# Kernel tuning notes

Measured on AMD Instinct MI355X. Metric: run time of the kernel, lower is better.

## Reference

```python
import jax, jax.numpy as jnp
import numpy as np

EPS = 1e-12  # torch F.normalize default eps


def _l2norm(x):
    n = jnp.sqrt(jnp.sum(x * x, axis=-1, keepdims=True))
    return x / jnp.maximum(n, EPS)


def setup_inputs() -> dict:
    key = jax.random.key(0)
    ks = jax.random.split(key, 8)
    B, T, V = 4, 2048, 512
    C, H, NB = 512, 4, 64
    return {
        "x": jax.random.normal(ks[0], (B, T, V), dtype=jnp.float32),
        "basis": jax.random.normal(ks[1], (V, 2 * NB), dtype=jnp.float32),
        "shared_q_w": jax.random.normal(ks[2], (V, C), dtype=jnp.float32) * 0.02,
        "shared_k_w": jax.random.normal(ks[3], (V, C), dtype=jnp.float32) * 0.02,
        "v_coeffs": jax.random.normal(ks[4], (C, 2 * NB), dtype=jnp.float32) * 0.02,
        "o_coeffs": jax.random.normal(ks[5], (C, 2 * NB), dtype=jnp.float32) * 0.02,
        "decay_logits": jnp.linspace(1.0, 5.0, H, dtype=jnp.float32),
        "out_scale": jnp.float32(0.1),
    }


def reference(x, basis, shared_q_w, shared_k_w, v_coeffs, o_coeffs, decay_logits, out_scale):
    B, T, V = x.shape
    H = decay_logits.shape[0]
    C = shared_q_w.shape[1]
    D = C // H

    v_w = basis @ v_coeffs.T  # [V, C]
    o_w = basis @ o_coeffs.T  # [V, C]

    q = _l2norm(x @ shared_q_w)  # [B, T, C]
    k = _l2norm(x @ shared_k_w)
    v = x @ v_w

    # [B, H, T, D]
    q = q.reshape(B, T, H, D).transpose(0, 2, 1, 3)
    k = k.reshape(B, T, H, D).transpose(0, 2, 1, 3)
    v = v.reshape(B, T, H, D).transpose(0, 2, 1, 3)

    scores = jnp.einsum("bhqd,bhkd->bhqk", q, k)  # [B, H, T, T]

    decay = jax.nn.sigmoid(decay_logits)  # [H]
    pos = jnp.arange(T)
    diff = pos[None, :] - pos[:, None]  # diff[i, j] = j - i
    mask = (diff > 0).astype(scores.dtype)  # [T, T]
    expo = jnp.clip(diff.astype(jnp.float32) - 1.0, 0.0, None)  # [T, T]
    decay_w = (decay[:, None, None] ** expo[None]) * mask[None]  # [H, T, T]

    scores = scores * decay_w[None].astype(scores.dtype)
    retrieved = jnp.einsum("bhqk,bhkd->bhqd", scores, v)  # [B, H, T, D]
    retrieved = retrieved.transpose(0, 2, 1, 3).reshape(B, T, C)
    return retrieved @ o_w.T * out_scale  # [B, T, V]
```

## Files before the change

### kernel.cpp

```cpp
#include <hip/hip_runtime.h>
#include <hip/hip_bf16.h>

#define BB 4
#define TT 2048
#define VV 512
#define CC 512
#define HH 4
#define DD 128
#define NB2 128
#define NROWS (BB*TT)
#define QC 64
#define NCH (TT/QC)
#define SST 66
#define EPS 1e-12f

typedef __attribute__((ext_vector_type(8))) short bf16x8;
typedef __attribute__((ext_vector_type(4))) float f32x4;
typedef unsigned short u16;

__device__ __forceinline__ void gl_lds16(const void* g, void* l) {
    __builtin_amdgcn_global_load_lds(
        (const __attribute__((address_space(1))) unsigned int*)g,
        (__attribute__((address_space(3))) unsigned int*)l, 16, 0, 0);
}
__device__ __forceinline__ u16 f2bu(float x) {
    __hip_bfloat16 h = __float2bfloat16(x);
    return *reinterpret_cast<u16*>(&h);
}
__device__ __forceinline__ float bu2f(u16 u) {
    __hip_bfloat16 h = *reinterpret_cast<__hip_bfloat16*>(&u);
    return __bfloat162float(h);
}
__device__ __forceinline__ uint4 pack8(float4 a, float4 b, float s) {
    u16 h[8] = {f2bu(a.x * s), f2bu(a.y * s), f2bu(a.z * s), f2bu(a.w * s),
                f2bu(b.x * s), f2bu(b.y * s), f2bu(b.z * s), f2bu(b.w * s)};
    return *(uint4*)h;
}

#define P4_TR  512
#define P4_Z   16
#define P4_WG  32
__global__ __launch_bounds__(256) void prep_all4(
    const float* __restrict__ qw, const float* __restrict__ kw,
    const float* __restrict__ basis, const float* __restrict__ v_coeffs,
    const float* __restrict__ o_coeffs, const float* __restrict__ out_scale,
    u16* __restrict__ wq, u16* __restrict__ wk,
    u16* __restrict__ v_wT, u16* __restrict__ o_ws, float* __restrict__ norms)
{
    __shared__ __align__(16) union {
        float tile[32][33];
        struct { u16 A[4096]; u16 B[4096]; } w;
    } sm;
    const int bi = blockIdx.x, t = threadIdx.x;
    if (bi < P4_TR) {
        int id = bi;
        const int z = id >> 8; id &= 255;
        const float* in = z ? kw : qw;
        u16* outT = z ? wk : wq;
        const int bx = (id & 15) * 32, by = (id >> 4) * 32;
        const int tx = t & 31, ty = t >> 5;
        #pragma unroll
        for (int r = 0; r < 32; r += 8)
            sm.tile[ty + r][tx] = in[(size_t)(by + ty + r) * CC + bx + tx];
        __syncthreads();
        #pragma unroll
        for (int r = 0; r < 32; r += 8)
            outT[(size_t)(bx + ty + r) * VV + by + tx] = f2bu(sm.tile[tx][ty + r]);
    } else if (bi < P4_TR + P4_Z) {
        int idx = (bi - P4_TR) * 256 + t;
        ((float4*)norms)[idx] = make_float4(0.f, 0.f, 0.f, 0.f);
    } else {
        int id = bi - (P4_TR + P4_Z);
        const int sec = id >> 4, rem = id & 15;
        const int m0 = (rem >> 2) * 128, n0 = (rem & 3) * 128;
        const float* Af = sec ? basis : v_coeffs;
        const float* Bf = sec ? o_coeffs : basis;
        u16* Cp = sec ? o_ws : v_wT;
        const float scB = sec ? out_scale[0] : 1.f;
        const int wave = t >> 6, lane = t & 63;
        const int qq = lane >> 4, l16 = lane & 15;
        const int wm = (wave >> 1) * 64, wn = (wave & 1) * 64;
        const int s0 = wave * 128 + lane, s1 = s0 + 64;
        const int r0 = s0 >> 2, c0 = ((s0 & 3) - (r0 >> 1)) & 3;
        const int r1 = s1 >> 2, c1 = ((s1 & 3) - (r1 >> 1)) & 3;
        f32x4 acc[4][4];
        #pragma unroll
        for (int i = 0; i < 4; ++i)
            #pragma unroll
            for (int j = 0; j < 4; ++j) acc[i][j] = (f32x4){0.f, 0.f, 0.f, 0.f};
        for (int k0 = 0; k0 < NB2; k0 += 32) {
            __syncthreads();
            {
                const float* p0 = Af + (size_t)(m0 + r0) * NB2 + k0 + c0 * 8;
                const float* p1 = Af + (size_t)(m0 + r1) * NB2 + k0 + c1 * 8;
                *(uint4*)&sm.w.A[s0 * 8] = pack8(((const float4*)p0)[0], ((const float4*)p0)[1], 1.f);
                *(uint4*)&sm.w.A[s1 * 8] = pack8(((const float4*)p1)[0], ((const float4*)p1)[1], 1.f);
                const float* q0 = Bf + (size_t)(n0 + r0) * NB2 + k0 + c0 * 8;
                const float* q1 = Bf + (size_t)(n0 + r1) * NB2 + k0 + c1 * 8;
                *(uint4*)&sm.w.B[s0 * 8] = pack8(((const float4*)q0)[0], ((const float4*)q0)[1], scB);
                *(uint4*)&sm.w.B[s1 * 8] = pack8(((const float4*)q1)[0], ((const float4*)q1)[1], scB);
            }
            __syncthreads();
            bf16x8 af[4], bfr[4];
            #pragma unroll
            for (int mt = 0; mt < 4; ++mt) {
                const int r = wm + mt * 16 + l16;
                af[mt] = *(const bf16x8*)&sm.w.A[(r * 4 + ((qq + (r >> 1)) & 3)) * 8];
            }
            #pragma unroll
            for (int nt = 0; nt < 4; ++nt) {
                const int r = wn + nt * 16 + l16;
                bfr[nt] = *(const bf16x8*)&sm.w.B[(r * 4 + ((qq + (r >> 1)) & 3)) * 8];
            }
            #pragma unroll
            for (int mt = 0; mt < 4; ++mt)
                #pragma unroll
                for (int nt = 0; nt < 4; ++nt)
                    acc[mt][nt] = __builtin_amdgcn_mfma_f32_16x16x32_bf16(
                        af[mt], bfr[nt], acc[mt][nt], 0, 0, 0);
        }
        #pragma unroll
        for (int mt = 0; mt < 4; ++mt)
            #pragma unroll
            for (int rr = 0; rr < 4; ++rr) {
                int grow = m0 + wm + mt * 16 + qq * 4 + rr;
                #pragma unroll
                for (int nt = 0; nt < 4; ++nt)
                    Cp[(size_t)grow * 512 + n0 + wn + nt * 16 + l16] = f2bu(acc[mt][nt][rr]);
            }
    }
}

__global__ __launch_bounds__(256) void gemm_qkv3(
    const float* __restrict__ x, const u16* __restrict__ wcat,
    u16* __restrict__ qo, u16* __restrict__ ko, u16* __restrict__ vo,
    float* __restrict__ norms)
{
    __shared__ __align__(16) u16 As[8192];
    __shared__ __align__(16) u16 Bs[8192];
    const int t = threadIdx.x;
    const int wave = t >> 6, lane = t & 63;
    const int qq = lane >> 4, l16 = lane & 15;
    const int bid = blockIdx.x;
    const int fid = (bid & 7) * 96 + (bid >> 3);
    const int mx = fid % 12;
    const int sec = mx >> 2;
    const int n0 = (mx & 3) * 128;
    const int m0 = (fid / 12) * 128;
    const int wm = (wave >> 1) * 64, wn = (wave & 1) * 64;
    const int K = VV;
    const u16* Bt = wcat + (size_t)sec * VV * CC;

    const int s0 = wave * 128 + lane, s1 = s0 + 64;
    const int r0_ = s0 >> 2, c0_ = ((s0 & 3) - (r0_ >> 1)) & 3;
    const int r1_ = s1 >> 2, c1_ = ((s1 & 3) - (r1_ >> 1)) & 3;
    const float* gax0 = x + (size_t)(m0 + r0_) * K + c0_ * 8;
    const float* gax1 = x + (size_t)(m0 + r1_) * K + c1_ * 8;
    const u16* gb0 = Bt + (size_t)(n0 + r0_) * K + c0_ * 8;
    const u16* gb1 = Bt + (size_t)(n0 + r1_) * K + c1_ * 8;
    const int lo0 = (wave * 128) * 8, lo1 = lo0 + 512;

    {
        float4 a0 = ((const float4*)gax0)[0], a1 = ((const float4*)gax0)[1];
        float4 b0 = ((const float4*)gax1)[0], b1 = ((const float4*)gax1)[1];
        *(uint4*)&As[s0 * 8] = pack8(a0, a1, 1.f);
        *(uint4*)&As[s1 * 8] = pack8(b0, b1, 1.f);
    }
    gl_lds16(gb0, Bs + lo0);
    gl_lds16(gb1, Bs + lo1);
    float4 na0 = ((const float4*)(gax0 + 32))[0];
    float4 na1 = ((const float4*)(gax0 + 32))[1];
    float4 nb0 = ((const float4*)(gax1 + 32))[0];
    float4 nb1 = ((const float4*)(gax1 + 32))[1];

    f32x4 acc[4][4];
    #pragma unroll
    for (int i = 0; i < 4; ++i)
        #pragma unroll
        for (int j = 0; j < 4; ++j) acc[i][j] = (f32x4){0.f, 0.f, 0.f, 0.f};

    int ib = 0;
    for (int k0 = 0; k0 < K; k0 += 32, ib ^= 1) {
        __syncthreads();
        if (k0 + 32 < K) {
            *(uint4*)&As[(ib ^ 1) * 4096 + s0 * 8] = pack8(na0, na1, 1.f);
            *(uint4*)&As[(ib ^ 1) * 4096 + s1 * 8] = pack8(nb0, nb1, 1.f);
            gl_lds16(gb0 + k0 + 32, Bs + (ib ^ 1) * 4096 + lo0);
            gl_lds16(gb1 + k0 + 32, Bs + (ib ^ 1) * 4096 + lo1);
        }
        if (k0 + 64 < K) {
            na0 = ((const float4*)(gax0 + k0 + 64))[0];
            na1 = ((const float4*)(gax0 + k0 + 64))[1];
            nb0 = ((const float4*)(gax1 + k0 + 64))[0];
            nb1 = ((const float4*)(gax1 + k0 + 64))[1];
        }
        const u16* Ac = As + ib * 4096;
        const u16* Bc = Bs + ib * 4096;
        bf16x8 af[4], bfr[4];
        #pragma unroll
        for (int mt = 0; mt < 4; ++mt) {
            const int r = wm + mt * 16 + l16;
            af[mt] = *(const bf16x8*)&Ac[(r * 4 + ((qq + (r >> 1)) & 3)) * 8];
        }
        #pragma unroll
        for (int nt = 0; nt < 4; ++nt) {
            const int r = wn + nt * 16 + l16;
            bfr[nt] = *(const bf16x8*)&Bc[(r * 4 + ((qq + (r >> 1)) & 3)) * 8];
        }
        #pragma unroll
        for (int mt = 0; mt < 4; ++mt)
            #pragma unroll
            for (int nt = 0; nt < 4; ++nt)
                acc[mt][nt] = __builtin_amdgcn_mfma_f32_16x16x32_bf16(
                    af[mt], bfr[nt], acc[mt][nt], 0, 0, 0);
    }

    u16* outp = sec == 0 ? qo : (sec == 1 ? ko : vo);
    #pragma unroll
    for (int mt = 0; mt < 4; ++mt)
        #pragma unroll
        for (int r = 0; r < 4; ++r) {
            int grow = m0 + wm + mt * 16 + qq * 4 + r;
            #pragma unroll
            for (int nt = 0; nt < 4; ++nt)
                outp[(size_t)grow * CC + n0 + wn + nt * 16 + l16] =
                    f2bu(acc[mt][nt][r]);
        }
    if (sec < 2) {
        float* np = sec == 0 ? norms : norms + NROWS;
        #pragma unroll
        for (int mt = 0; mt < 4; ++mt)
            #pragma unroll
            for (int r = 0; r < 4; ++r) {
                float s = 0.f;
                #pragma unroll
                for (int nt = 0; nt < 4; ++nt) {
                    float v = acc[mt][nt][r];
                    s = fmaf(v, v, s);
                }
                s += __shfl_xor(s, 1, 64);
                s += __shfl_xor(s, 2, 64);
                s += __shfl_xor(s, 4, 64);
                s += __shfl_xor(s, 8, 64);
                if (l16 == 0)
                    atomicAdd(&np[m0 + wm + mt * 16 + qq * 4 + r], s);
            }
    }
}

__global__ __launch_bounds__(256) void state_local(
    const u16* __restrict__ kb, const u16* __restrict__ vb,
    const float* __restrict__ norms_k, const float* __restrict__ dlog,
    u16* __restrict__ statesb)
{
    __shared__ __align__(16) u16 vT[DD][SST];
    __shared__ __align__(16) u16 kT[DD][SST];
    const int c = blockIdx.x, bh = blockIdx.y;
    const int b = bh >> 2, h = bh & 3;
    const float lam = 1.f / (1.f + __expf(-dlog[h]));
    const float l2lam = log2f(lam);
    const int t = threadIdx.x;
    const int row0 = b * TT + c * QC;
    const size_t gbase = (size_t)row0 * CC + h * DD;

    {
        const int j2 = t & 31, d0 = (t >> 5) * 16;
        const int jj0 = 2 * j2, jj1 = jj0 + 1;
        const float w0 = exp2f((float)jj0 * l2lam);
        const float w1 = exp2f((float)jj1 * l2lam);
        const float rk0 = 1.f / fmaxf(sqrtf(norms_k[row0 + jj0]), EPS);
        const float rk1 = 1.f / fmaxf(sqrtf(norms_k[row0 + jj1]), EPS);
        u16 k0a[16], k1a[16], v0a[16], v1a[16];
        const u16* k0p = kb + gbase + (size_t)jj0 * CC + d0;
        const u16* k1p = kb + gbase + (size_t)jj1 * CC + d0;
        const u16* v0p = vb + gbase + (size_t)jj0 * CC + d0;
        const u16* v1p = vb + gbase + (size_t)jj1 * CC + d0;
        *(uint4*)&k0a[0] = *(const uint4*)k0p; *(uint4*)&k0a[8] = *(const uint4*)(k0p + 8);
        *(uint4*)&k1a[0] = *(const uint4*)k1p; *(uint4*)&k1a[8] = *(const uint4*)(k1p + 8);
        *(uint4*)&v0a[0] = *(const uint4*)v0p; *(uint4*)&v0a[8] = *(const uint4*)(v0p + 8);
        *(uint4*)&v1a[0] = *(const uint4*)v1p; *(uint4*)&v1a[8] = *(const uint4*)(v1p + 8);
        #pragma unroll
        for (int i = 0; i < 16; ++i) {
            unsigned int kw = (unsigned int)f2bu(bu2f(k0a[i]) * rk0)
                            | ((unsigned int)f2bu(bu2f(k1a[i]) * rk1) << 16);
            *(unsigned int*)&kT[d0 + i][jj0] = kw;
            unsigned int vw = (unsigned int)f2bu(bu2f(v0a[i]) * w0)
                            | ((unsigned int)f2bu(bu2f(v1a[i]) * w1) << 16);
            *(unsigned int*)&vT[d0 + i][jj0] = vw;
        }
    }
    __syncthreads();

    const int wave = t >> 6, lane = t & 63;
    const int quad = lane >> 4, l16 = lane & 15;
    f32x4 acc[2][8];
    #pragma unroll
    for (int i = 0; i < 2; ++i)
        #pragma unroll
        for (int j = 0; j < 8; ++j) acc[i][j] = (f32x4){0.f, 0.f, 0.f, 0.f};

    #pragma unroll
    for (int s = 0; s < 2; ++s) {
        bf16x8 af[2];
        #pragma unroll
        for (int mt = 0; mt < 2; ++mt)
            af[mt] = *(const bf16x8*)&vT[wave * 32 + mt * 16 + l16][s * 32 + quad * 8];
        #pragma unroll
        for (int nt = 0; nt < 8; ++nt) {
            bf16x8 bk = *(const bf16x8*)&kT[nt * 16 + l16][s * 32 + quad * 8];
            #pragma unroll
            for (int mt = 0; mt < 2; ++mt)
                acc[mt][nt] = __builtin_amdgcn_mfma_f32_16x16x32_bf16(
                    af[mt], bk, acc[mt][nt], 0, 0, 0);
        }
    }
    u16* so = statesb + ((size_t)(bh * NCH + c) << 14);
    #pragma unroll
    for (int mt = 0; mt < 2; ++mt)
        #pragma unroll
        for (int rr = 0; rr < 4; ++rr) {
            const int d = wave * 32 + mt * 16 + quad * 4 + rr;
            #pragma unroll
            for (int nt = 0; nt < 8; ++nt)
                so[(size_t)d * DD + nt * 16 + l16] = f2bu(acc[mt][nt][rr]);
        }
}

__global__ __launch_bounds__(256) void state_combine512(
    const float* __restrict__ dlog, u16* __restrict__ statesb)
{
    const int bh = blockIdx.x >> 5, part = blockIdx.x & 31;
    const int h = bh & 3;
    const float lam = 1.f / (1.f + __expf(-dlog[h]));
    const float lamQ = exp2f((float)QC * log2f(lam));
    const int t = threadIdx.x;
    unsigned int* pb = (unsigned int*)(statesb + ((size_t)(bh * NCH) << 14))
                       + part * 256 + t;
    unsigned int vals[NCH];
    #pragma unroll
    for (int c = 0; c < NCH; ++c) vals[c] = pb[(size_t)c * 8192];
    float run0 = 0.f, run1 = 0.f;
    #pragma unroll
    for (int c = NCH - 1; c >= 0; --c) {
        float t0 = bu2f((u16)(vals[c] & 0xffffu));
        float t1 = bu2f((u16)(vals[c] >> 16));
        pb[(size_t)c * 8192] = (unsigned int)f2bu(run0)
                             | ((unsigned int)f2bu(run1) << 16);
        run0 = fmaf(lamQ, run0, t0);
        run1 = fmaf(lamQ, run1, t1);
    }
}

__global__ __launch_bounds__(256) void attention_fused(
    const u16* __restrict__ qb, const u16* __restrict__ kb,
    const u16* __restrict__ vb, const u16* __restrict__ statesb,
    const float* __restrict__ norms, const float* __restrict__ dlog,
    u16* __restrict__ retb)
{
    __shared__ __align__(16) u16 qks[2 * QC * DD];
    __shared__ __align__(16) u16 vsT[DD][SST];
    __shared__ __align__(16) u16 ss[QC][SST];
    __shared__ float rql[QC], rkl[QC];

    const int c = blockIdx.x, bh = blockIdx.y;
    const int b = bh >> 2, h = bh & 3;
    const float lam = 1.f / (1.f + __expf(-dlog[h]));
    const float l2lam = log2f(lam);
    const int t = threadIdx.x;
    const int row0 = b * TT + c * QC;
    const size_t base = (size_t)row0 * CC + h * DD;

    const int wave = t >> 6, lane = t & 63;
    const int quad = lane >> 4, l16 = lane & 15;
    const int r0 = wave * 16;

    {
        const int lrow = lane >> 4, cch = lane & 15;
        #pragma unroll
        for (int u = 0; u < 4; ++u) {
            const int R = wave * 16 + u * 4;
            const int gr = R + lrow;
            const int cq = (cch - gr) & 15;
            gl_lds16(qb + base + (size_t)gr * CC + cq * 8, &qks[R * DD]);
            gl_lds16(kb + base + (size_t)gr * CC + cq * 8, &qks[(QC + R) * DD]);
        }
    }
    if (t < QC)            rql[t]      = 1.f / fmaxf(sqrtf(norms[row0 + t]), EPS);
    else if (t < 2 * QC)   rkl[t - QC] = 1.f / fmaxf(sqrtf(norms[NROWS + row0 + t - QC]), EPS);
    {
        const int j2 = t & 31, d0 = (t >> 5) * 16;
        const u16* v0 = vb + base + (size_t)(2 * j2) * CC + d0;
        const u16* v1 = v0 + CC;
        uint4 a0 = *(const uint4*)v0;
        uint4 a1 = *(const uint4*)(v0 + 8);
        uint4 b0 = *(const uint4*)v1;
        uint4 b1 = *(const uint4*)(v1 + 8);
        const u16* ap0 = (const u16*)&a0; const u16* ap1 = (const u16*)&a1;
        const u16* bp0 = (const u16*)&b0; const u16* bp1 = (const u16*)&b1;
        #pragma unroll
        for (int i = 0; i < 8; ++i) {
            *(unsigned int*)&vsT[d0 + i][2 * j2] =
                (unsigned int)ap0[i] | ((unsigned int)bp0[i] << 16);
            *(unsigned int*)&vsT[d0 + 8 + i][2 * j2] =
                (unsigned int)ap1[i] | ((unsigned int)bp1[i] << 16);
        }
    }
    __syncthreads();

    bf16x8 aq[4];
    #pragma unroll
    for (int kq = 0; kq < 4; ++kq) {
        const int r = r0 + l16;
        aq[kq] = *(const bf16x8*)&qks[r * DD + ((kq * 4 + quad + r) & 15) * 8];
    }

    f32x4 accs[4];
    #pragma unroll
    for (int nt = 0; nt < 4; ++nt) accs[nt] = (f32x4){0.f, 0.f, 0.f, 0.f};
    #pragma unroll
    for (int nt = 0; nt < 4; ++nt)
        #pragma unroll
        for (int kq = 0; kq < 4; ++kq) {
            const int rk_ = nt * 16 + l16;
            bf16x8 bk = *(const bf16x8*)&qks[(QC + rk_) * DD + ((kq * 4 + quad + rk_) & 15) * 8];
            accs[nt] = __builtin_amdgcn_mfma_f32_16x16x32_bf16(aq[kq], bk, accs[nt], 0, 0, 0);
        }

    #pragma unroll
    for (int nt = 0; nt < 4; ++nt) {
        const int j = nt * 16 + l16;
        const float rkj = rkl[j];
        #pragma unroll
        for (int rr = 0; rr < 4; ++rr) {
            const int i = r0 + quad * 4 + rr;
            const int di = j - i;
            float p = (di > 0) ? accs[nt][rr] * exp2f((float)(di - 1) * l2lam) * rkj : 0.f;
            ss[i][j] = f2bu(p);
        }
    }
    __syncthreads();

    const u16* sb = statesb + ((size_t)(bh * NCH + c) << 14);
    {
        const int drow = lane >> 4, cch = lane & 15;
        #pragma unroll
        for (int u = 0; u < 8; ++u) {
            const int D = wave * 32 + u * 4;
            const int gd = D + drow;
            const int cq = (cch - gd) & 15;
            gl_lds16(sb + (size_t)gd * DD + cq * 8, &qks[D * DD]);
        }
    }
    bf16x8 ap[2];
    #pragma unroll
    for (int kj = 0; kj < 2; ++kj)
        ap[kj] = *(const bf16x8*)&ss[r0 + l16][kj * 32 + quad * 8];
    f32x4 accd[8];
    #pragma unroll
    for (int nt = 0; nt < 8; ++nt) accd[nt] = (f32x4){0.f, 0.f, 0.f, 0.f};
    #pragma unroll
    for (int nt = 0; nt < 8; ++nt)
        #pragma unroll
        for (int kj = 0; kj < 2; ++kj) {
            bf16x8 bv = *(const bf16x8*)&vsT[nt * 16 + l16][kj * 32 + quad * 8];
            accd[nt] = __builtin_amdgcn_mfma_f32_16x16x32_bf16(ap[kj], bv, accd[nt], 0, 0, 0);
        }
    __syncthreads();

    f32x4 accc[8];
    #pragma unroll
    for (int nt = 0; nt < 8; ++nt) accc[nt] = (f32x4){0.f, 0.f, 0.f, 0.f};
    #pragma unroll
    for (int nt = 0; nt < 8; ++nt)
        #pragma unroll
        for (int kq = 0; kq < 4; ++kq) {
            const int d = nt * 16 + l16;
            bf16x8 bs_ = *(const bf16x8*)&qks[d * DD + ((kq * 4 + quad + d) & 15) * 8];
            accc[nt] = __builtin_amdgcn_mfma_f32_16x16x32_bf16(aq[kq], bs_, accc[nt], 0, 0, 0);
        }

    u16* rb = retb + (size_t)row0 * CC + h * DD;
    #pragma unroll
    for (int rr = 0; rr < 4; ++rr) {
        const int ii = r0 + quad * 4 + rr;
        const float wrow = exp2f((float)(QC - 1 - ii) * l2lam);
        const float rq = rql[ii];
        #pragma unroll
        for (int nt = 0; nt < 8; ++nt) {
            float val = (accd[nt][rr] + wrow * accc[nt][rr]) * rq;
            rb[(size_t)ii * CC + nt * 16 + l16] = f2bu(val);
        }
    }
}

__global__ __launch_bounds__(256) void gemm_out64(
    const u16* __restrict__ A, const u16* __restrict__ Bt, float* __restrict__ C)
{
    __shared__ __align__(16) u16 As[4096];
    __shared__ __align__(16) u16 Bs[8192];
    const int t = threadIdx.x;
    const int wave = t >> 6, lane = t & 63;
    const int qq = lane >> 4, l16 = lane & 15;
    const int bid = blockIdx.x;
    const int fid = (bid & 7) * 64 + (bid >> 3);
    const int m0 = (fid >> 2) * 64, n0 = (fid & 3) * 128;
    const int wm = (wave >> 1) * 32, wn = (wave & 1) * 64;
    const int N = VV, K = CC;

    const int sA = wave * 64 + lane;
    const int rA = sA >> 2, cA = ((sA & 3) - (rA >> 1)) & 3;
    const int sB0 = wave * 128 + lane, sB1 = sB0 + 64;
    const int rB0 = sB0 >> 2, cB0 = ((sB0 & 3) - (rB0 >> 1)) & 3;
    const int rB1 = sB1 >> 2, cB1 = ((sB1 & 3) - (rB1 >> 1)) & 3;
    const u16* ga  = A  + (size_t)(m0 + rA) * K + cA * 8;
    const u16* gb0 = Bt + (size_t)(n0 + rB0) * K + cB0 * 8;
    const u16* gb1 = Bt + (size_t)(n0 + rB1) * K + cB1 * 8;
    const int loA = wave * 512, loB0 = wave * 1024, loB1 = wave * 1024 + 512;

    gl_lds16(ga, As + loA);
    gl_lds16(gb0, Bs + loB0);
    gl_lds16(gb1, Bs + loB1);

    f32x4 acc[2][4];
    #pragma unroll
    for (int i = 0; i < 2; ++i)
        #pragma unroll
        for (int j = 0; j < 4; ++j) acc[i][j] = (f32x4){0.f, 0.f, 0.f, 0.f};

    int ib = 0;
    for (int k0 = 0; k0 < K; k0 += 32, ib ^= 1) {
        __syncthreads();
        if (k0 + 32 < K) {
            gl_lds16(ga + k0 + 32,  As + (ib ^ 1) * 2048 + loA);
            gl_lds16(gb0 + k0 + 32, Bs + (ib ^ 1) * 4096 + loB0);
            gl_lds16(gb1 + k0 + 32, Bs + (ib ^ 1) * 4096 + loB1);
        }
        const u16* Ac = As + ib * 2048;
        const u16* Bc = Bs + ib * 4096;
        bf16x8 af[2], bfr[4];
        #pragma unroll
        for (int mt = 0; mt < 2; ++mt) {
            const int r = wm + mt * 16 + l16;
            af[mt] = *(const bf16x8*)&Ac[(r * 4 + ((qq + (r >> 1)) & 3)) * 8];
        }
        #pragma unroll
        for (int nt = 0; nt < 4; ++nt) {
            const int r = wn + nt * 16 + l16;
            bfr[nt] = *(const bf16x8*)&Bc[(r * 4 + ((qq + (r >> 1)) & 3)) * 8];
        }
        #pragma unroll
        for (int mt = 0; mt < 2; ++mt)
            #pragma unroll
            for (int nt = 0; nt < 4; ++nt)
                acc[mt][nt] = __builtin_amdgcn_mfma_f32_16x16x32_bf16(
                    af[mt], bfr[nt], acc[mt][nt], 0, 0, 0);
    }
    #pragma unroll
    for (int mt = 0; mt < 2; ++mt)
        #pragma unroll
        for (int r = 0; r < 4; ++r) {
            int grow = m0 + wm + mt * 16 + qq * 4 + r;
            #pragma unroll
            for (int nt = 0; nt < 4; ++nt)
                C[(size_t)grow * N + n0 + wn + nt * 16 + l16] = acc[mt][nt][r];
        }
}

extern "C" void kernel_launch(void* const* d_in, const int* in_sizes, int n_in,
                              void* d_out, int out_size, void* d_ws, size_t ws_size,
                              hipStream_t stream) {
    const float* x         = (const float*)d_in[0];
    const float* basis     = (const float*)d_in[1];
    const float* qw        = (const float*)d_in[2];
    const float* kw        = (const float*)d_in[3];
    const float* v_coeffs  = (const float*)d_in[4];
    const float* o_coeffs  = (const float*)d_in[5];
    const float* dlog      = (const float*)d_in[6];
    const float* out_scale = (const float*)d_in[7];
    float* out             = (float*)d_out;

    u16* p = (u16*)d_ws;
    u16* qb      = p;
    u16* kb      = qb + (size_t)NROWS * CC;
    u16* vb      = kb + (size_t)NROWS * CC;
    u16* statesb = vb + (size_t)NROWS * CC;
    u16* retb    = statesb + (size_t)BB * HH * NCH * DD * DD;
    u16* wcat    = retb + (size_t)NROWS * CC;
    u16* o_ws    = wcat + 3 * (size_t)VV * CC;
    float* norms = (float*)(o_ws + (size_t)VV * CC);

    prep_all4<<<P4_TR + P4_Z + P4_WG, 256, 0, stream>>>(
        qw, kw, basis, v_coeffs, o_coeffs, out_scale,
        wcat, wcat + (size_t)VV * CC, wcat + 2 * (size_t)VV * CC, o_ws, norms);
    gemm_qkv3<<<768, 256, 0, stream>>>(x, wcat, qb, kb, vb, norms);
    state_local     <<<dim3(NCH, BB * HH), 256, 0, stream>>>(kb, vb, norms + NROWS,
                                                             dlog, statesb);
    state_combine512<<<BB * HH * 32, 256, 0, stream>>>(dlog, statesb);
    attention_fused <<<dim3(NCH, BB * HH), 256, 0, stream>>>(qb, kb, vb, statesb,
                                                             norms, dlog, retb);
    gemm_out64<<<512, 256, 0, stream>>>(retb, o_ws, out);
}
```

Baseline: 148.2 us.

## Load QKV GEMM operands directly from global into MFMA registers, dropping LDS staging

The fused QKV projection GEMM no longer stages A (fp32 x converted to bf16) and B tiles through double-buffered shared memory with barriers. Each lane now loads its MFMA fragments straight from global memory into registers and prefetches the next k-step in registers. This removes LDS traffic and __syncthreads, but gives up cross-wave reuse: each x row is reloaded by both column waves and each weight row by both row waves, and the global loads are less coalesced.

```diff
diff --git a/kernel.cpp b/kernel.cpp
--- a/kernel.cpp
+++ b/kernel.cpp
@@ -136,8 +136,6 @@
     u16* __restrict__ qo, u16* __restrict__ ko, u16* __restrict__ vo,
     float* __restrict__ norms)
 {
-    __shared__ __align__(16) u16 As[8192];
-    __shared__ __align__(16) u16 Bs[8192];
     const int t = threadIdx.x;
     const int wave = t >> 6, lane = t & 63;
     const int qq = lane >> 4, l16 = lane & 15;
@@ -148,30 +146,16 @@
     const int n0 = (mx & 3) * 128;
     const int m0 = (fid / 12) * 128;
     const int wm = (wave >> 1) * 64, wn = (wave & 1) * 64;
-    const int K = VV;
     const u16* Bt = wcat + (size_t)sec * VV * CC;
 
-    const int s0 = wave * 128 + lane, s1 = s0 + 64;
-    const int r0_ = s0 >> 2, c0_ = ((s0 & 3) - (r0_ >> 1)) & 3;
-    const int r1_ = s1 >> 2, c1_ = ((s1 & 3) - (r1_ >> 1)) & 3;
-    const float* gax0 = x + (size_t)(m0 + r0_) * K + c0_ * 8;
-    const float* gax1 = x + (size_t)(m0 + r1_) * K + c1_ * 8;
-    const u16* gb0 = Bt + (size_t)(n0 + r0_) * K + c0_ * 8;
-    const u16* gb1 = Bt + (size_t)(n0 + r1_) * K + c1_ * 8;
-    const int lo0 = (wave * 128) * 8, lo1 = lo0 + 512;
-
-    {
-        float4 a0 = ((const float4*)gax0)[0], a1 = ((const float4*)gax0)[1];
-        float4 b0 = ((const float4*)gax1)[0], b1 = ((const float4*)gax1)[1];
-        *(uint4*)&As[s0 * 8] = pack8(a0, a1, 1.f);
-        *(uint4*)&As[s1 * 8] = pack8(b0, b1, 1.f);
-    }
-    gl_lds16(gb0, Bs + lo0);
-    gl_lds16(gb1, Bs + lo1);
-    float4 na0 = ((const float4*)(gax0 + 32))[0];
-    float4 na1 = ((const float4*)(gax0 + 32))[1];
-    float4 nb0 = ((const float4*)(gax1 + 32))[0];
-    float4 nb1 = ((const float4*)(gax1 + 32))[1];
+    const float* pa[4];
+    const u16*   pb[4];
+    #pragma unroll
+    for (int mt = 0; mt < 4; ++mt)
+        pa[mt] = x + (size_t)(m0 + wm + mt * 16 + l16) * VV + qq * 8;
+    #pragma unroll
+    for (int nt = 0; nt < 4; ++nt)
+        pb[nt] = Bt + (size_t)(n0 + wn + nt * 16 + l16) * VV + qq * 8;
 
     f32x4 acc[4][4];
     #pragma unroll
@@ -179,33 +163,36 @@
         #pragma unroll
         for (int j = 0; j < 4; ++j) acc[i][j] = (f32x4){0.f, 0.f, 0.f, 0.f};
 
-    int ib = 0;
-    for (int k0 = 0; k0 < K; k0 += 32, ib ^= 1) {
-        __syncthreads();
-        if (k0 + 32 < K) {
-            *(uint4*)&As[(ib ^ 1) * 4096 + s0 * 8] = pack8(na0, na1, 1.f);
-            *(uint4*)&As[(ib ^ 1) * 4096 + s1 * 8] = pack8(nb0, nb1, 1.f);
-            gl_lds16(gb0 + k0 + 32, Bs + (ib ^ 1) * 4096 + lo0);
-            gl_lds16(gb1 + k0 + 32, Bs + (ib ^ 1) * 4096 + lo1);
-        }
-        if (k0 + 64 < K) {
-            na0 = ((const float4*)(gax0 + k0 + 64))[0];
-            na1 = ((const float4*)(gax0 + k0 + 64))[1];
-            nb0 = ((const float4*)(gax1 + k0 + 64))[0];
-            nb1 = ((const float4*)(gax1 + k0 + 64))[1];
-        }
-        const u16* Ac = As + ib * 4096;
-        const u16* Bc = Bs + ib * 4096;
+    float4 a0[4], a1[4];
+    uint4  bq[4];
+    #pragma unroll
+    for (int mt = 0; mt < 4; ++mt) {
+        a0[mt] = ((const float4*)pa[mt])[0];
+        a1[mt] = ((const float4*)pa[mt])[1];
+    }
+    #pragma unroll
+    for (int nt = 0; nt < 4; ++nt)
+        bq[nt] = *(const uint4*)pb[nt];
+
+    for (int k0 = 0; k0 < VV; k0 += 32) {
         bf16x8 af[4], bfr[4];
         #pragma unroll
         for (int mt = 0; mt < 4; ++mt) {
-            const int r = wm + mt * 16 + l16;
-            af[mt] = *(const bf16x8*)&Ac[(r * 4 + ((qq + (r >> 1)) & 3)) * 8];
-        }
-        #pragma unroll
-        for (int nt = 0; nt < 4; ++nt) {
-            const int r = wn + nt * 16 + l16;
-            bfr[nt] = *(const bf16x8*)&Bc[(r * 4 + ((qq + (r >> 1)) & 3)) * 8];
+            uint4 p = pack8(a0[mt], a1[mt], 1.f);
+            af[mt] = *(bf16x8*)&p;
+        }
+        #pragma unroll
+        for (int nt = 0; nt < 4; ++nt)
+            bfr[nt] = *(bf16x8*)&bq[nt];
+        if (k0 + 32 < VV) {
+            #pragma unroll
+            for (int mt = 0; mt < 4; ++mt) {
+                a0[mt] = ((const float4*)(pa[mt] + k0 + 32))[0];
+                a1[mt] = ((const float4*)(pa[mt] + k0 + 32))[1];
+            }
+            #pragma unroll
+            for (int nt = 0; nt < 4; ++nt)
+                bq[nt] = *(const uint4*)(pb[nt] + k0 + 32);
         }
         #pragma unroll
         for (int mt = 0; mt < 4; ++mt)
```

New measurement: 192.3 us. +29.8%, slower.
